# Kernel tuning notes

Measured on AMD Instinct MI355X. Metric: run time of the kernel, lower is better.

## Reference

```python
import jax, jax.numpy as jnp
import numpy as np

NUM_HEADS = 12
THETA = 10000.0

def apply_rope(x, pos, theta):
    # x: [B, H, S, d_k]; pos: [S]
    d_k = x.shape[-1]
    inv_freq = theta ** (-jnp.arange(0, d_k, 2, dtype=jnp.float32) / d_k)  # [d_k/2]
    ang = pos[:, None].astype(jnp.float32) * inv_freq[None, :]             # [S, d_k/2]
    cos, sin = jnp.cos(ang), jnp.sin(ang)
    x1, x2 = x[..., ::2], x[..., 1::2]
    out_even = x1 * cos - x2 * sin
    out_odd = x1 * sin + x2 * cos
    # interleave back to [..., d_k]
    return jnp.stack([out_even, out_odd], axis=-1).reshape(x.shape)

def setup_inputs() -> dict:
    key = jax.random.key(0)
    ks = jax.random.split(key, 5)
    B, S, D = 1, 4096, 768
    x = jax.random.normal(ks[0], (B, S, D), dtype=jnp.float32)
    scale = 0.02
    Wq = jax.random.normal(ks[1], (D, D), dtype=jnp.float32) * scale
    Wk = jax.random.normal(ks[2], (D, D), dtype=jnp.float32) * scale
    Wv = jax.random.normal(ks[3], (D, D), dtype=jnp.float32) * scale
    Wo = jax.random.normal(ks[4], (D, D), dtype=jnp.float32) * scale
    return {"x": x, "Wq": Wq, "Wk": Wk, "Wv": Wv, "Wo": Wo}

def reference(x, Wq, Wk, Wv, Wo):
    B, S, D = x.shape
    H = NUM_HEADS
    d_k = D // H
    # projections (torch Linear: y = x @ W.T, no bias)
    Q = x @ Wq.T
    K = x @ Wk.T
    V = x @ Wv.T
    # [B, S, H*d_k] -> [B, H, S, d_k]
    def split_heads(t):
        return t.reshape(B, S, H, d_k).transpose(0, 2, 1, 3)
    Q, K, V = split_heads(Q), split_heads(K), split_heads(V)
    pos = jnp.arange(S)
    Q = apply_rope(Q, pos, THETA)
    K = apply_rope(K, pos, THETA)
    scores = jnp.einsum('bhnd,bhmd->bhnm', Q, K) * (d_k ** -0.5)  # [B,H,S,S]
    causal = jnp.tril(jnp.ones((S, S), dtype=bool))
    scores = jnp.where(causal, scores, -jnp.inf)
    attn = jax.nn.softmax(scores, axis=-1)
    out = jnp.einsum('bhnm,bhmd->bhnd', attn, V)  # [B,H,S,d_k]
    out = out.transpose(0, 2, 1, 3).reshape(B, S, D)
    return out @ Wo.T
```

## Files before the change

### kernel.cpp

```cpp
#include <hip/hip_runtime.h>
#include <hip/hip_bf16.h>
#include <cstdint>

typedef __bf16 bf16x8 __attribute__((ext_vector_type(8)));
typedef float f32x4 __attribute__((ext_vector_type(4)));
typedef float f32x16 __attribute__((ext_vector_type(16)));

static constexpr int S = 4096;
static constexpr int D = 768;
static constexpr int DK = 64;

__device__ __forceinline__ unsigned short f2bf(float f) {
  unsigned u = __float_as_uint(f);
  u = (u + 0x7fffu + ((u >> 16) & 1u)) >> 16;
  return (unsigned short)u;
}

__global__ __launch_bounds__(256) void cvt5_kernel(
    const float* __restrict__ x, const float* __restrict__ wq,
    const float* __restrict__ wk, const float* __restrict__ wv,
    const float* __restrict__ wo,
    unsigned short* __restrict__ xb, unsigned short* __restrict__ wqb,
    unsigned short* __restrict__ wkb, unsigned short* __restrict__ wvb,
    unsigned short* __restrict__ wob) {
  int i = blockIdx.x * blockDim.x + threadIdx.x;
  constexpr int NX4 = (S * D) / 4;
  constexpr int NW4 = (D * D) / 4;
  const float* src;
  unsigned short* dst;
  int off;
  if (i < NX4)               { src = x;  dst = xb;  off = i; }
  else if (i < NX4 + NW4)    { src = wq; dst = wqb; off = i - NX4; }
  else if (i < NX4 + 2*NW4)  { src = wk; dst = wkb; off = i - NX4 - NW4; }
  else if (i < NX4 + 3*NW4)  { src = wv; dst = wvb; off = i - NX4 - 2*NW4; }
  else                       { src = wo; dst = wob; off = i - NX4 - 3*NW4; }
  float4 v = reinterpret_cast<const float4*>(src)[off];
  ushort4 o;
  o.x = f2bf(v.x); o.y = f2bf(v.y); o.z = f2bf(v.z); o.w = f2bf(v.w);
  reinterpret_cast<ushort4*>(dst)[off] = o;
}

__global__ __launch_bounds__(256) void ropetab_kernel(float2* __restrict__ tab) {
  int idx = blockIdx.x * blockDim.x + threadIdx.x;
  int s = idx >> 5, i = idx & 31;
  float freq = expf(-(float)(2 * i) * (9.210340371976184f / 64.0f));
  float si, c;
  sincosf((float)s * freq, &si, &c);
  tab[idx] = make_float2(c, si);
}

__global__ __launch_bounds__(256) void qkv_gemm_kernel(
    const unsigned short* __restrict__ xb,
    const unsigned short* __restrict__ Wall,
    const float2* __restrict__ tab,
    unsigned short* __restrict__ Qh,
    unsigned short* __restrict__ Kf,
    unsigned short* __restrict__ Vf) {
  __shared__ alignas(16) unsigned short At[2][128 * 64];
  __shared__ alignas(16) unsigned short Bt[2][128 * 64];

  const int t = threadIdx.x;
  const int lane = t & 63;
  const int lr = lane & 15;
  const int hi = lane >> 4;
  const int wave = t >> 6;
  const int wr = wave >> 1, wc = wave & 1;
  const int row0 = blockIdx.x * 128;
  const int n0 = blockIdx.y * 128;

  const int trow = t >> 3;
  const int tc8  = (t & 7) * 8;
  const int tsw8 = (((t & 7) ^ (trow & 7)) * 8);
  const int sx = lr & 7;

  f32x4 acc[4][4] = {};

  auto stage = [&](int buf, int k0) {
#pragma unroll
    for (int i = 0; i < 4; ++i) {
      __builtin_amdgcn_global_load_lds(
          (const __attribute__((address_space(1))) void*)(
              xb + (size_t)(row0 + trow + 32 * i) * 768 + k0 + tsw8),
          (__attribute__((address_space(3))) void*)(&At[buf][(trow + 32 * i) * 64 + tc8]),
          16, 0, 0);
      __builtin_amdgcn_global_load_lds(
          (const __attribute__((address_space(1))) void*)(
              Wall + (size_t)(n0 + trow + 32 * i) * 768 + k0 + tsw8),
          (__attribute__((address_space(3))) void*)(&Bt[buf][(trow + 32 * i) * 64 + tc8]),
          16, 0, 0);
    }
  };

  stage(0, 0);
  __syncthreads();

#pragma unroll
  for (int ts = 0; ts < 12; ++ts) {
    const int cur = ts & 1;
    if (ts + 1 < 12) stage(cur ^ 1, (ts + 1) * 64);
#pragma unroll
    for (int kk = 0; kk < 2; ++kk) {
      const int csw = ((kk * 4 + hi) ^ sx) * 8;
      bf16x8 a[4], b[4];
#pragma unroll
      for (int rf = 0; rf < 4; ++rf)
        a[rf] = *reinterpret_cast<const bf16x8*>(
            &At[cur][(wr * 64 + rf * 16 + lr) * 64 + csw]);
#pragma unroll
      for (int nf = 0; nf < 4; ++nf)
        b[nf] = *reinterpret_cast<const bf16x8*>(
            &Bt[cur][(wc * 64 + nf * 16 + lr) * 64 + csw]);
#pragma unroll
      for (int rf = 0; rf < 4; ++rf)
#pragma unroll
        for (int nf = 0; nf < 4; ++nf)
          acc[rf][nf] = __builtin_amdgcn_mfma_f32_16x16x32_bf16(a[rf], b[nf], acc[rf][nf], 0, 0, 0);
    }
    __syncthreads();
  }

  const int z = n0 / 768;

  if (z < 2) {
#pragma unroll
    for (int nf = 0; nf < 4; ++nf) {
      const int c = n0 - z * 768 + wc * 64 + nf * 16 + lr;
      const int hh = c >> 6;
      const int dk = c & 63;
      const int ii = dk >> 1;
#pragma unroll
      for (int rf = 0; rf < 4; ++rf) {
        const int jrow = row0 + wr * 64 + rf * 16 + hi * 4;
#pragma unroll
        for (int j = 0; j < 4; ++j) {
          float v = acc[rf][nf][j];
          const int s = jrow + j;
          float pv = __shfl_xor(v, 1);
          float2 cs = tab[(size_t)s * 32 + ii];
          v = (dk & 1) ? (pv * cs.y + v * cs.x) : (v * cs.x - pv * cs.y);
          if (z == 0) {
            Qh[((size_t)hh * S + s) * DK + dk] = f2bf(v * 0.18033688f);
          } else {
            const size_t koff = ((size_t)hh * 128 + (s >> 5)) * 2048 +
                                (size_t)(dk >> 4) * 512 + ((dk >> 3) & 1) * 256 +
                                (s & 31) * 8 + (dk & 7);
            Kf[koff] = f2bf(v);
          }
        }
      }
    }
  } else {
#pragma unroll
    for (int nf = 0; nf < 4; ++nf) {
      const int c = n0 - 1536 + wc * 64 + nf * 16 + lr;
      const int hh = c >> 6;
      const int dv = c & 63;
#pragma unroll
      for (int rf = 0; rf < 4; ++rf) {
        const int jrow = row0 + wr * 64 + rf * 16 + hi * 4;
#pragma unroll
        for (int j = 0; j < 4; ++j) {
          const int s = jrow + j;
          const size_t voff = ((size_t)hh * 256 + (s >> 4)) * 1024 +
                              (size_t)(dv >> 5) * 512 + (dv & 31) * 16 +
                              ((s >> 3) & 1) * 8 + (s & 7);
          Vf[voff] = f2bf(acc[rf][nf][j]);
        }
      }
    }
  }
}

__global__ __launch_bounds__(256) void attn_kernel(
    const unsigned short* __restrict__ Qh,
    const unsigned short* __restrict__ Kf,
    const unsigned short* __restrict__ Vf,
    unsigned short* __restrict__ AO) {
  const int w = blockIdx.x * 192 + blockIdx.y;
  const int h = w >> 7;
  const int qt = 127 - (w & 127);
  const int wave = threadIdx.x >> 6;
  const int lane = threadIdx.x & 63;
  const int lq = lane & 31;
  const int hi2 = lane >> 5;
  const int q0w = qt * 32;
  const int qg = q0w + lq;

  const unsigned short* Qp = Qh + ((size_t)h * S + qg) * DK + hi2 * 8;
  const unsigned short* Kfp = Kf + (size_t)h * (S * DK) + hi2 * 256 + lq * 8;
  const unsigned short* Vfp = Vf + (size_t)h * (S * DK) + lq * 16 + hi2 * 8;

  bf16x8 qf[4];
#pragma unroll
  for (int ks = 0; ks < 4; ++ks)
    qf[ks] = *reinterpret_cast<const bf16x8*>(Qp + ks * 16);

  f32x16 acc0 = {}, acc1 = {};
  float lsum[16];
#pragma unroll
  for (int r = 0; r < 16; ++r) lsum[r] = 0.f;

  const int kvmax = ((q0w + 31) >> 6) << 6;
  const int kvfirst = 64 * wave;

  bf16x8 kaA[2][4], vbA[2][4], kaB[2][4], vbB[2][4];

  auto loadkv = [&](bf16x8 (&ka)[2][4], bf16x8 (&vb)[2][4], int kvb) {
    const unsigned short* Kn = Kfp + ((size_t)(kvb >> 5)) * 2048;
#pragma unroll
    for (int tt = 0; tt < 2; ++tt)
#pragma unroll
      for (int ks = 0; ks < 4; ++ks)
        ka[tt][ks] = *reinterpret_cast<const bf16x8*>(Kn + (size_t)tt * 2048 + ks * 512);
#pragma unroll
    for (int dvh = 0; dvh < 2; ++dvh)
#pragma unroll
      for (int ks = 0; ks < 4; ++ks)
        vb[dvh][ks] = *reinterpret_cast<const bf16x8*>(
            Vfp + ((size_t)(kvb >> 4) + ks) * 1024 + dvh * 512);
  };

  auto process = [&](bf16x8 (&ka)[2][4], bf16x8 (&vb)[2][4], int kv0) {
    f32x16 s0 = {}, s1 = {};
#pragma unroll
    for (int ks = 0; ks < 4; ++ks) {
      s0 = __builtin_amdgcn_mfma_f32_32x32x16_bf16(ka[0][ks], qf[ks], s0, 0, 0, 0);
      s1 = __builtin_amdgcn_mfma_f32_32x32x16_bf16(ka[1][ks], qf[ks], s1, 0, 0, 0);
    }

    if ((kv0 + 63) > q0w) {
#pragma unroll
      for (int r = 0; r < 16; ++r) {
        const int kvr = kv0 + (r & 3) + 8 * (r >> 2) + 4 * hi2;
        if (kvr > qg) s0[r] = -1e30f;
        if (kvr + 32 > qg) s1[r] = -1e30f;
      }
    }

#pragma unroll
    for (int r = 0; r < 16; ++r) {
      float e0, e1;
      asm("v_exp_f32 %0, %1" : "=v"(e0) : "v"(s0[r]));
      asm("v_exp_f32 %0, %1" : "=v"(e1) : "v"(s1[r]));
      s0[r] = e0;
      s1[r] = e1;
      lsum[r] += e0 + e1;
    }

    bf16x8 pa[4];
#pragma unroll
    for (int ks = 0; ks < 4; ++ks) {
      const int a4 = 8 * (ks & 1);
      unsigned X01, X23, Y01, Y23;
      if (ks < 2) {
        asm("v_cvt_pk_bf16_f32 %0, %1, %2" : "=v"(X01) : "v"(s0[a4 + 0]), "v"(s0[a4 + 1]));
        asm("v_cvt_pk_bf16_f32 %0, %1, %2" : "=v"(X23) : "v"(s0[a4 + 2]), "v"(s0[a4 + 3]));
        asm("v_cvt_pk_bf16_f32 %0, %1, %2" : "=v"(Y01) : "v"(s0[a4 + 4]), "v"(s0[a4 + 5]));
        asm("v_cvt_pk_bf16_f32 %0, %1, %2" : "=v"(Y23) : "v"(s0[a4 + 6]), "v"(s0[a4 + 7]));
      } else {
        asm("v_cvt_pk_bf16_f32 %0, %1, %2" : "=v"(X01) : "v"(s1[a4 + 0]), "v"(s1[a4 + 1]));
        asm("v_cvt_pk_bf16_f32 %0, %1, %2" : "=v"(X23) : "v"(s1[a4 + 2]), "v"(s1[a4 + 3]));
        asm("v_cvt_pk_bf16_f32 %0, %1, %2" : "=v"(Y01) : "v"(s1[a4 + 4]), "v"(s1[a4 + 5]));
        asm("v_cvt_pk_bf16_f32 %0, %1, %2" : "=v"(Y23) : "v"(s1[a4 + 6]), "v"(s1[a4 + 7]));
      }
      asm volatile("v_permlane32_swap_b32 %0, %1" : "+v"(X01), "+v"(Y01));
      asm volatile("v_permlane32_swap_b32 %0, %1" : "+v"(X23), "+v"(Y23));
      union { unsigned u[4]; bf16x8 v; } P;
      P.u[0] = X01; P.u[1] = X23; P.u[2] = Y01; P.u[3] = Y23;
      pa[ks] = P.v;
    }

#pragma unroll
    for (int ks = 0; ks < 4; ++ks) {
      acc0 = __builtin_amdgcn_mfma_f32_32x32x16_bf16(pa[ks], vb[0][ks], acc0, 0, 0, 0);
      acc1 = __builtin_amdgcn_mfma_f32_32x32x16_bf16(pa[ks], vb[1][ks], acc1, 0, 0, 0);
    }
  };

  if (kvfirst <= kvmax) {
    loadkv(kaA, vbA, kvfirst);
    int kv0 = kvfirst;
    while (true) {
      const int kvn = kv0 + 256;
      const bool haveB = kvn <= kvmax;
      if (haveB) loadkv(kaB, vbB, kvn);
      process(kaA, vbA, kv0);
      if (!haveB) break;
      kv0 = kvn;
      const int kvn2 = kv0 + 256;
      const bool haveA = kvn2 <= kvmax;
      if (haveA) loadkv(kaA, vbA, kvn2);
      process(kaB, vbB, kv0);
      if (!haveA) break;
      kv0 = kvn2;
    }
  }

#pragma unroll
  for (int off = 8; off > 0; off >>= 1)
#pragma unroll
    for (int r = 0; r < 8; ++r)
      if (r < off) lsum[r] += lsum[r + off];
  const float l_ = lsum[0] + __shfl_xor(lsum[0], 32);

  __shared__ float llds[4][32];
  __shared__ float obuf[4][64][33];

  if (hi2 == 0) llds[wave][lq] = l_;
#pragma unroll
  for (int r = 0; r < 16; ++r) {
    obuf[wave][lane][r]      = acc0[r];
    obuf[wave][lane][r + 16] = acc1[r];
  }
  __syncthreads();

  const float Ltot = llds[0][lq] + llds[1][lq] + llds[2][lq] + llds[3][lq];
  const float linv = 1.0f / Ltot;

#pragma unroll
  for (int rr = 0; rr < 4; ++rr) {
    const int r = wave * 4 + rr;
    float v0 = obuf[0][lane][r] + obuf[1][lane][r] + obuf[2][lane][r] + obuf[3][lane][r];
    float v1 = obuf[0][lane][r + 16] + obuf[1][lane][r + 16] +
               obuf[2][lane][r + 16] + obuf[3][lane][r + 16];
    const int row = (r & 3) + 8 * (r >> 2) + 4 * hi2;
    const float li = __shfl(linv, row);
    const size_t s = q0w + row;
    AO[s * D + h * DK + lq]      = f2bf(v0 * li);
    AO[s * D + h * DK + 32 + lq] = f2bf(v1 * li);
  }
}

__global__ __launch_bounds__(256) void oproj_kernel(
    const unsigned short* __restrict__ AO,
    const unsigned short* __restrict__ Wob,
    float* __restrict__ out) {
  __shared__ alignas(16) unsigned short At[2][128 * 64];
  __shared__ alignas(16) unsigned short Bt[2][128 * 64];

  const int t = threadIdx.x;
  const int lane = t & 63;
  const int lr = lane & 15;
  const int hi = lane >> 4;
  const int wave = t >> 6;
  const int wr = wave >> 1, wc = wave & 1;
  const int row0 = blockIdx.x * 128;
  const int n0 = blockIdx.y * 128;

  const int trow = t >> 3;
  const int tc8  = (t & 7) * 8;
  const int tsw8 = (((t & 7) ^ (trow & 7)) * 8);
  const int sx = lr & 7;

  f32x4 acc[4][4] = {};

  auto stage = [&](int buf, int k0) {
#pragma unroll
    for (int i = 0; i < 4; ++i) {
      __builtin_amdgcn_global_load_lds(
          (const __attribute__((address_space(1))) void*)(
              AO + (size_t)(row0 + trow + 32 * i) * 768 + k0 + tsw8),
          (__attribute__((address_space(3))) void*)(&At[buf][(trow + 32 * i) * 64 + tc8]),
          16, 0, 0);
      __builtin_amdgcn_global_load_lds(
          (const __attribute__((address_space(1))) void*)(
              Wob + (size_t)(n0 + trow + 32 * i) * 768 + k0 + tsw8),
          (__attribute__((address_space(3))) void*)(&Bt[buf][(trow + 32 * i) * 64 + tc8]),
          16, 0, 0);
    }
  };

  stage(0, 0);
  __syncthreads();

#pragma unroll
  for (int ts = 0; ts < 12; ++ts) {
    const int cur = ts & 1;
    if (ts + 1 < 12) stage(cur ^ 1, (ts + 1) * 64);
#pragma unroll
    for (int kk = 0; kk < 2; ++kk) {
      const int csw = ((kk * 4 + hi) ^ sx) * 8;
      bf16x8 a[4], b[4];
#pragma unroll
      for (int rf = 0; rf < 4; ++rf)
        a[rf] = *reinterpret_cast<const bf16x8*>(
            &At[cur][(wr * 64 + rf * 16 + lr) * 64 + csw]);
#pragma unroll
      for (int nf = 0; nf < 4; ++nf)
        b[nf] = *reinterpret_cast<const bf16x8*>(
            &Bt[cur][(wc * 64 + nf * 16 + lr) * 64 + csw]);
#pragma unroll
      for (int rf = 0; rf < 4; ++rf)
#pragma unroll
        for (int nf = 0; nf < 4; ++nf)
          acc[rf][nf] = __builtin_amdgcn_mfma_f32_16x16x32_bf16(a[rf], b[nf], acc[rf][nf], 0, 0, 0);
    }
    __syncthreads();
  }

#pragma unroll
  for (int rf = 0; rf < 4; ++rf) {
    const int jrow = row0 + wr * 64 + rf * 16 + hi * 4;
#pragma unroll
    for (int nf = 0; nf < 4; ++nf) {
      const int cn = n0 + wc * 64 + nf * 16 + lr;
#pragma unroll
      for (int j = 0; j < 4; ++j)
        out[(size_t)(jrow + j) * D + cn] = acc[rf][nf][j];
    }
  }
}

extern "C" void kernel_launch(void* const* d_in, const int* in_sizes, int n_in,
                              void* d_out, int out_size, void* d_ws, size_t ws_size,
                              hipStream_t stream) {
  const float* x  = (const float*)d_in[0];
  const float* Wq = (const float*)d_in[1];
  const float* Wk = (const float*)d_in[2];
  const float* Wv = (const float*)d_in[3];
  const float* Wo = (const float*)d_in[4];
  float* out = (float*)d_out;

  char* ws = (char*)d_ws;
  unsigned short* xb  = (unsigned short*)(ws + 0);
  unsigned short* Wqb = (unsigned short*)(ws + 6291456);
  unsigned short* Wkb = (unsigned short*)(ws + 7471104);
  unsigned short* Wvb = (unsigned short*)(ws + 8650752);
  unsigned short* Wob = (unsigned short*)(ws + 9830400);
  unsigned short* Qh  = (unsigned short*)(ws + 11010048);
  unsigned short* Kf  = (unsigned short*)(ws + 17301504);
  unsigned short* Vf  = (unsigned short*)(ws + 23592960);
  unsigned short* AO  = (unsigned short*)(ws + 29884416);
  float2* tab = (float2*)(ws + 29884416);

  cvt5_kernel<<<5376, 256, 0, stream>>>(x, Wq, Wk, Wv, Wo, xb, Wqb, Wkb, Wvb, Wob);
  ropetab_kernel<<<512, 256, 0, stream>>>(tab);
  qkv_gemm_kernel<<<dim3(32, 18), 256, 0, stream>>>(xb, Wqb, tab, Qh, Kf, Vf);
  attn_kernel<<<dim3(8, 192), 256, 0, stream>>>(Qh, Kf, Vf, AO);
  oproj_kernel<<<dim3(32, 6), 256, 0, stream>>>(AO, Wob, out);
}
```

Before: 121.1 us.

## Shrink attention register and LDS footprint with single-buffered KV prefetch and split reduction

Replaces the double-buffered K/V register prefetch with a single K buffer prefetched after the QK MFMAs and V loaded at the top of each iteration. It also halves the cross-wave output reduction buffer in shared memory by reducing acc0 and acc1 in two passes with extra barriers. The aim is to cut VGPR and LDS usage so more waves can be resident. The cost is less latency hiding for V loads and two additional __syncthreads in the epilogue.

```diff
diff --git a/kernel.cpp b/kernel.cpp
--- a/kernel.cpp
+++ b/kernel.cpp
@@ -203,29 +203,39 @@
   const int kvmax = ((q0w + 31) >> 6) << 6;
   const int kvfirst = 64 * wave;
 
-  bf16x8 kaA[2][4], vbA[2][4], kaB[2][4], vbB[2][4];
-
-  auto loadkv = [&](bf16x8 (&ka)[2][4], bf16x8 (&vb)[2][4], int kvb) {
-    const unsigned short* Kn = Kfp + ((size_t)(kvb >> 5)) * 2048;
+  bf16x8 ka[2][4];
+  if (kvfirst <= kvmax) {
+    const unsigned short* K0 = Kfp + ((size_t)(kvfirst >> 5)) * 2048;
 #pragma unroll
     for (int tt = 0; tt < 2; ++tt)
 #pragma unroll
       for (int ks = 0; ks < 4; ++ks)
-        ka[tt][ks] = *reinterpret_cast<const bf16x8*>(Kn + (size_t)tt * 2048 + ks * 512);
+        ka[tt][ks] = *reinterpret_cast<const bf16x8*>(K0 + (size_t)tt * 2048 + ks * 512);
+  }
+
+  for (int kv0 = kvfirst; kv0 <= kvmax; kv0 += 256) {
+    bf16x8 vb[2][4];
 #pragma unroll
     for (int dvh = 0; dvh < 2; ++dvh)
 #pragma unroll
       for (int ks = 0; ks < 4; ++ks)
         vb[dvh][ks] = *reinterpret_cast<const bf16x8*>(
-            Vfp + ((size_t)(kvb >> 4) + ks) * 1024 + dvh * 512);
-  };
-
-  auto process = [&](bf16x8 (&ka)[2][4], bf16x8 (&vb)[2][4], int kv0) {
+            Vfp + ((size_t)(kv0 >> 4) + ks) * 1024 + dvh * 512);
+
     f32x16 s0 = {}, s1 = {};
 #pragma unroll
     for (int ks = 0; ks < 4; ++ks) {
       s0 = __builtin_amdgcn_mfma_f32_32x32x16_bf16(ka[0][ks], qf[ks], s0, 0, 0, 0);
       s1 = __builtin_amdgcn_mfma_f32_32x32x16_bf16(ka[1][ks], qf[ks], s1, 0, 0, 0);
+    }
+
+    if ((kv0 + 256) <= kvmax) {
+      const unsigned short* Kn = Kfp + ((size_t)((kv0 + 256) >> 5)) * 2048;
+#pragma unroll
+      for (int tt = 0; tt < 2; ++tt)
+#pragma unroll
+        for (int ks = 0; ks < 4; ++ks)
+          ka[tt][ks] = *reinterpret_cast<const bf16x8*>(Kn + (size_t)tt * 2048 + ks * 512);
     }
 
     if ((kv0 + 63) > q0w) {
@@ -275,25 +285,6 @@
       acc0 = __builtin_amdgcn_mfma_f32_32x32x16_bf16(pa[ks], vb[0][ks], acc0, 0, 0, 0);
       acc1 = __builtin_amdgcn_mfma_f32_32x32x16_bf16(pa[ks], vb[1][ks], acc1, 0, 0, 0);
     }
-  };
-
-  if (kvfirst <= kvmax) {
-    loadkv(kaA, vbA, kvfirst);
-    int kv0 = kvfirst;
-    while (true) {
-      const int kvn = kv0 + 256;
-      const bool haveB = kvn <= kvmax;
-      if (haveB) loadkv(kaB, vbB, kvn);
-      process(kaA, vbA, kv0);
-      if (!haveB) break;
-      kv0 = kvn;
-      const int kvn2 = kv0 + 256;
-      const bool haveA = kvn2 <= kvmax;
-      if (haveA) loadkv(kaA, vbA, kvn2);
-      process(kaB, vbB, kv0);
-      if (!haveA) break;
-      kv0 = kvn2;
-    }
   }
 
 #pragma unroll
@@ -304,29 +295,37 @@
   const float l_ = lsum[0] + __shfl_xor(lsum[0], 32);
 
   __shared__ float llds[4][32];
-  __shared__ float obuf[4][64][33];
+  __shared__ float obuf[4][64][17];
 
   if (hi2 == 0) llds[wave][lq] = l_;
-#pragma unroll
-  for (int r = 0; r < 16; ++r) {
-    obuf[wave][lane][r]      = acc0[r];
-    obuf[wave][lane][r + 16] = acc1[r];
-  }
+
+#pragma unroll
+  for (int r = 0; r < 16; ++r) obuf[wave][lane][r] = acc0[r];
   __syncthreads();
 
   const float Ltot = llds[0][lq] + llds[1][lq] + llds[2][lq] + llds[3][lq];
   const float linv = 1.0f / Ltot;
 
+  float v0[4];
 #pragma unroll
   for (int rr = 0; rr < 4; ++rr) {
     const int r = wave * 4 + rr;
-    float v0 = obuf[0][lane][r] + obuf[1][lane][r] + obuf[2][lane][r] + obuf[3][lane][r];
-    float v1 = obuf[0][lane][r + 16] + obuf[1][lane][r + 16] +
-               obuf[2][lane][r + 16] + obuf[3][lane][r + 16];
+    v0[rr] = obuf[0][lane][r] + obuf[1][lane][r] + obuf[2][lane][r] + obuf[3][lane][r];
+  }
+  __syncthreads();
+
+#pragma unroll
+  for (int r = 0; r < 16; ++r) obuf[wave][lane][r] = acc1[r];
+  __syncthreads();
+
+#pragma unroll
+  for (int rr = 0; rr < 4; ++rr) {
+    const int r = wave * 4 + rr;
+    const float v1 = obuf[0][lane][r] + obuf[1][lane][r] + obuf[2][lane][r] + obuf[3][lane][r];
     const int row = (r & 3) + 8 * (r >> 2) + 4 * hi2;
     const float li = __shfl(linv, row);
     const size_t s = q0w + row;
-    AO[s * D + h * DK + lq]      = f2bf(v0 * li);
+    AO[s * D + h * DK + lq]      = f2bf(v0[rr] * li);
     AO[s * D + h * DK + 32 + lq] = f2bf(v1 * li);
   }
 }
```

New measurement: 107.7 us. -11.1%, faster.
